# Performance work log

Measured on AMD Instinct MI355X. Metric: run time of the kernel, lower is better.

Reference implementation:

```python
import jax, jax.numpy as jnp
import numpy as np

EPS = 1e-07
NEG_DIAG = -10.0
HDCE_GAMMA = 1.0

def l2_normalize(x):
    # norm = (sum(x^2, axis=1))^(1/2); out = x / (norm + 1e-7)
    norm = jnp.sqrt(jnp.sum(x * x, axis=1, keepdims=True))
    return x / (norm + EPS)

def setup_inputs() -> dict:
    key = jax.random.key(0)
    k1, k2, k3 = jax.random.split(key, 3)
    N, D, DG = 4096, 256, 256
    feat_q = jax.random.normal(k1, (N, D), dtype=jnp.float32)
    feat_k = jax.random.normal(k2, (N, D), dtype=jnp.float32)
    feat_g = jax.random.normal(k3, (N, DG), dtype=jnp.float32)
    return {"feat_q": feat_q, "feat_k": feat_k, "feat_g": feat_g}

def reference(feat_q, feat_k, feat_g):
    N = feat_q.shape[0]
    fq = l2_normalize(feat_q)  # computed in original but unused for weight_out
    fk = l2_normalize(feat_k)
    fg = l2_normalize(feat_g)
    # batched self-similarity with batch_dim_for_bmm = 1 -> [1, N, N]
    spatial_k = jnp.einsum('nd,md->nm', fk, fk)[None]
    spatial_g = jnp.einsum('nd,md->nm', fg, fg)[None]
    spatial_kg = (spatial_k + 1.0 + EPS) / (spatial_g + 1.0 + EPS)
    diag = jnp.eye(N, dtype=bool)[None]  # [1, N, N]
    weight_seed = jnp.where(diag, NEG_DIAG, spatial_kg)
    weight_out = jax.nn.softmax(weight_seed / HDCE_GAMMA, axis=2)
    wmax = jnp.max(weight_out, axis=2, keepdims=True)
    return weight_out / wmax
```

## Files before the change

### kernel.cpp

```cpp
#include <hip/hip_runtime.h>
#include <hip/hip_bf16.h>
#include <cmath>

typedef __attribute__((ext_vector_type(8))) short short8;
typedef __attribute__((ext_vector_type(4))) float f32x4;

#define EPS_F 1e-7f
#define NEG_DIAG_F -10.0f

__device__ __forceinline__ unsigned enc_f32(float f) {
    unsigned u = __float_as_uint(f);
    return (u & 0x80000000u) ? ~u : (u | 0x80000000u);
}
__device__ __forceinline__ float dec_f32(unsigned u) {
    return (u & 0x80000000u) ? __uint_as_float(u ^ 0x80000000u) : __uint_as_float(~u);
}

__device__ __forceinline__ void gload_lds16(const void* gptr, void* ldsptr) {
    __builtin_amdgcn_global_load_lds(
        (const __attribute__((address_space(1))) unsigned int*)gptr,
        (__attribute__((address_space(3))) unsigned int*)ldsptr,
        16, 0, 0);
}

__global__ void norm_cast_kernel(const float* __restrict__ fk, const float* __restrict__ fg,
                                 __hip_bfloat16* __restrict__ fkb, __hip_bfloat16* __restrict__ fgb,
                                 unsigned* __restrict__ rowmax, int N, int D) {
    int n = blockIdx.x;
    int t = threadIdx.x;
    float xk = fk[(size_t)n * D + t];
    float xg = fg[(size_t)n * D + t];
    float sk = xk * xk, sg = xg * xg;
#pragma unroll
    for (int off = 32; off > 0; off >>= 1) {
        sk += __shfl_xor(sk, off, 64);
        sg += __shfl_xor(sg, off, 64);
    }
    __shared__ float lsk[4], lsg[4];
    int w = t >> 6, l = t & 63;
    if (l == 0) { lsk[w] = sk; lsg[w] = sg; }
    __syncthreads();
    sk = lsk[0] + lsk[1] + lsk[2] + lsk[3];
    sg = lsg[0] + lsg[1] + lsg[2] + lsg[3];
    float rkv = 1.0f / (sqrtf(sk) + EPS_F);
    float rgv = 1.0f / (sqrtf(sg) + EPS_F);
    fkb[(size_t)n * D + t] = __float2bfloat16(xk * rkv);
    fgb[(size_t)n * D + t] = __float2bfloat16(xg * rgv);
    if (t == 0) rowmax[n] = 0u;
}

#define BM 128
#define BN 128
#define BK 64
#define NTHREADS 512

__global__ __launch_bounds__(NTHREADS) void dual_gram_kernel(
    const __hip_bfloat16* __restrict__ fkb, const __hip_bfloat16* __restrict__ fgb,
    float* __restrict__ out, unsigned* __restrict__ rowmax, int N, int D) {

    __shared__ __align__(16) __hip_bfloat16 lAk[BM * BK];
    __shared__ __align__(16) __hip_bfloat16 lBk[BN * BK];
    __shared__ __align__(16) __hip_bfloat16 lAg[BM * BK];
    __shared__ __align__(16) __hip_bfloat16 lBg[BN * BK];

    int t = threadIdx.x;
    int ntiles = N / BN;
    int bid = blockIdx.x;
    int by = bid / ntiles, bx = bid % ntiles;
    int r0 = by * BM, c0 = bx * BN;

    int w = t >> 6, l = t & 63;
    int wr = w >> 2, wc = w & 3;
    int lr = l & 15, lg = l >> 4;

    f32x4 acck[4][2], accg[4][2];
    f32x4 zero = {0.f, 0.f, 0.f, 0.f};
#pragma unroll
    for (int m = 0; m < 4; ++m)
#pragma unroll
        for (int n = 0; n < 2; ++n) { acck[m][n] = zero; accg[m][n] = zero; }

    const size_t rowbytes = (size_t)D * 2;

    for (int k0 = 0; k0 < D; k0 += BK) {
#pragma unroll
        for (int c = 0; c < 2; ++c) {
            int o = (t + c * NTHREADS) * 16;
            int row = o >> 7;
            int csw = (o & 127) ^ ((row & 7) << 4);
            size_t goffA = (size_t)(r0 + row) * rowbytes + (size_t)k0 * 2 + csw;
            size_t goffB = (size_t)(c0 + row) * rowbytes + (size_t)k0 * 2 + csw;
            int ldsoff = (w << 10) + (c << 13);
            gload_lds16((const char*)fkb + goffA, (char*)lAk + ldsoff);
            gload_lds16((const char*)fkb + goffB, (char*)lBk + ldsoff);
            gload_lds16((const char*)fgb + goffA, (char*)lAg + ldsoff);
            gload_lds16((const char*)fgb + goffB, (char*)lBg + ldsoff);
        }
        __syncthreads();

#pragma unroll
        for (int kk = 0; kk < BK; kk += 32) {
            int kb = (kk + lg * 8) * 2;
            short8 ak[4], ag[4], bk2[2], bg2[2];
#pragma unroll
            for (int m = 0; m < 4; ++m) {
                int row = wr * 64 + m * 16 + lr;
                int o = (row << 7) + kb;
                o ^= ((row & 7) << 4);
                ak[m] = *(const short8*)((const char*)lAk + o);
                ag[m] = *(const short8*)((const char*)lAg + o);
            }
#pragma unroll
            for (int n = 0; n < 2; ++n) {
                int row = wc * 32 + n * 16 + lr;
                int o = (row << 7) + kb;
                o ^= ((row & 7) << 4);
                bk2[n] = *(const short8*)((const char*)lBk + o);
                bg2[n] = *(const short8*)((const char*)lBg + o);
            }
#pragma unroll
            for (int m = 0; m < 4; ++m)
#pragma unroll
                for (int n = 0; n < 2; ++n) {
                    acck[m][n] = __builtin_amdgcn_mfma_f32_16x16x32_bf16(ak[m], bk2[n], acck[m][n], 0, 0, 0);
                    accg[m][n] = __builtin_amdgcn_mfma_f32_16x16x32_bf16(ag[m], bg2[n], accg[m][n], 0, 0, 0);
                }
        }
        __syncthreads();
    }

    int gcoln[2];
#pragma unroll
    for (int n = 0; n < 2; ++n) gcoln[n] = c0 + wc * 32 + n * 16 + lr;

#pragma unroll
    for (int m = 0; m < 4; ++m) {
#pragma unroll
        for (int j = 0; j < 4; ++j) {
            int grow = r0 + wr * 64 + m * 16 + lg * 4 + j;
            float pm = NEG_DIAG_F;
#pragma unroll
            for (int n = 0; n < 2; ++n) {
                float dk = acck[m][n][j];
                float dg = accg[m][n][j];
                float s = (dk + 1.0f + EPS_F) / (dg + 1.0f + EPS_F);
                if (grow == gcoln[n]) s = NEG_DIAG_F;
                out[(size_t)grow * N + gcoln[n]] = s;
                pm = fmaxf(pm, s);
            }
#pragma unroll
            for (int off = 1; off < 16; off <<= 1)
                pm = fmaxf(pm, __shfl_xor(pm, off, 64));
            if (lr == 0) atomicMax(&rowmax[grow], enc_f32(pm));
        }
    }
}

__global__ void finalize_kernel(float* __restrict__ out, const unsigned* __restrict__ rowmax, int N) {
    size_t total = (size_t)N * N / 4;
    int cols4 = N / 4;
    size_t stride = (size_t)gridDim.x * blockDim.x;
    for (size_t i = (size_t)blockIdx.x * blockDim.x + threadIdx.x; i < total; i += stride) {
        float4 v = reinterpret_cast<float4*>(out)[i];
        int row = (int)(i / cols4);
        float m = dec_f32(rowmax[row]);
        v.x = __expf(v.x - m);
        v.y = __expf(v.y - m);
        v.z = __expf(v.z - m);
        v.w = __expf(v.w - m);
        reinterpret_cast<float4*>(out)[i] = v;
    }
}

extern "C" void kernel_launch(void* const* d_in, const int* in_sizes, int n_in,
                              void* d_out, int out_size, void* d_ws, size_t ws_size,
                              hipStream_t stream) {
    const float* fk = (const float*)d_in[1];
    const float* fg = (const float*)d_in[2];
    float* out = (float*)d_out;

    int N = (int)llround(sqrt((double)out_size));
    int D = in_sizes[1] / N;

    char* ws = (char*)d_ws;
    __hip_bfloat16* fkb = (__hip_bfloat16*)ws;
    __hip_bfloat16* fgb = (__hip_bfloat16*)(ws + (size_t)N * D * 2);
    unsigned* rowmax = (unsigned*)(ws + (size_t)N * D * 4);

    norm_cast_kernel<<<N, D, 0, stream>>>(fk, fg, fkb, fgb, rowmax, N, D);

    int nt = N / BN;
    dual_gram_kernel<<<nt * nt, NTHREADS, 0, stream>>>(fkb, fgb, out, rowmax, N, D);

    finalize_kernel<<<2048, 256, 0, stream>>>(out, rowmax, N);
}
```

Before: 77.71 us.

## Double-buffer gram tiles with BK=32, swizzle workgroup order, cheaper divide and indexing

Restructures the dual-gram main loop into a double-buffered LDS pipeline with BK=32. The next k-slice is prefetched via global_load_lds while MFMAs run on the current one, using a new XOR swizzle and precomputed LDS offsets. It also remaps block IDs so consecutive workgroups land on different tile rows, raises wave priority around MFMAs, and replaces the fp32 divide with a hardware reciprocal. The finalize row index now uses a shift, which is only correct when N/4 is a power of two, and the reciprocal slightly changes rounding.

```diff
diff --git a/kernel.cpp b/kernel.cpp
--- a/kernel.cpp
+++ b/kernel.cpp
@@ -51,21 +51,21 @@
 
 #define BM 128
 #define BN 128
-#define BK 64
+#define BK 32
 #define NTHREADS 512
+#define TILE_B (BM * BK * 2)
+#define BUF_B  (4 * TILE_B)
 
 __global__ __launch_bounds__(NTHREADS) void dual_gram_kernel(
     const __hip_bfloat16* __restrict__ fkb, const __hip_bfloat16* __restrict__ fgb,
     float* __restrict__ out, unsigned* __restrict__ rowmax, int N, int D) {
 
-    __shared__ __align__(16) __hip_bfloat16 lAk[BM * BK];
-    __shared__ __align__(16) __hip_bfloat16 lBk[BN * BK];
-    __shared__ __align__(16) __hip_bfloat16 lAg[BM * BK];
-    __shared__ __align__(16) __hip_bfloat16 lBg[BN * BK];
+    __shared__ __align__(16) char smem[2 * BUF_B];
 
     int t = threadIdx.x;
     int ntiles = N / BN;
-    int bid = blockIdx.x;
+    int nwg = ntiles * ntiles;
+    int bid = (blockIdx.x & 7) * (nwg >> 3) + (blockIdx.x >> 3);
     int by = bid / ntiles, bx = bid % ntiles;
     int r0 = by * BM, c0 = bx * BN;
 
@@ -73,6 +73,26 @@
     int wr = w >> 2, wc = w & 3;
     int lr = l & 15, lg = l >> 4;
 
+    int srow = t >> 2;
+    int sslot = t & 3;
+    int scsb = ((sslot ^ ((srow >> 1) & 3)) << 4);
+    const size_t rowbytes = (size_t)D * 2;
+    size_t gA = (size_t)(r0 + srow) * rowbytes + scsb;
+    size_t gB = (size_t)(c0 + srow) * rowbytes + scsb;
+    int ldst = t << 4;
+
+    int aoff[4], boff[2];
+#pragma unroll
+    for (int m = 0; m < 4; ++m) {
+        int row = wr * 64 + m * 16 + lr;
+        aoff[m] = row * 64 + (((lg ^ ((row >> 1) & 3))) << 4);
+    }
+#pragma unroll
+    for (int n = 0; n < 2; ++n) {
+        int row = wc * 32 + n * 16 + lr;
+        boff[n] = row * 64 + (((lg ^ ((row >> 1) & 3))) << 4);
+    }
+
     f32x4 acck[4][2], accg[4][2];
     f32x4 zero = {0.f, 0.f, 0.f, 0.f};
 #pragma unroll
@@ -80,52 +100,47 @@
 #pragma unroll
         for (int n = 0; n < 2; ++n) { acck[m][n] = zero; accg[m][n] = zero; }
 
-    const size_t rowbytes = (size_t)D * 2;
-
-    for (int k0 = 0; k0 < D; k0 += BK) {
-#pragma unroll
-        for (int c = 0; c < 2; ++c) {
-            int o = (t + c * NTHREADS) * 16;
-            int row = o >> 7;
-            int csw = (o & 127) ^ ((row & 7) << 4);
-            size_t goffA = (size_t)(r0 + row) * rowbytes + (size_t)k0 * 2 + csw;
-            size_t goffB = (size_t)(c0 + row) * rowbytes + (size_t)k0 * 2 + csw;
-            int ldsoff = (w << 10) + (c << 13);
-            gload_lds16((const char*)fkb + goffA, (char*)lAk + ldsoff);
-            gload_lds16((const char*)fkb + goffB, (char*)lBk + ldsoff);
-            gload_lds16((const char*)fgb + goffA, (char*)lAg + ldsoff);
-            gload_lds16((const char*)fgb + goffB, (char*)lBg + ldsoff);
-        }
-        __syncthreads();
-
-#pragma unroll
-        for (int kk = 0; kk < BK; kk += 32) {
-            int kb = (kk + lg * 8) * 2;
-            short8 ak[4], ag[4], bk2[2], bg2[2];
-#pragma unroll
-            for (int m = 0; m < 4; ++m) {
-                int row = wr * 64 + m * 16 + lr;
-                int o = (row << 7) + kb;
-                o ^= ((row & 7) << 4);
-                ak[m] = *(const short8*)((const char*)lAk + o);
-                ag[m] = *(const short8*)((const char*)lAg + o);
+    int ksteps = D / BK;
+
+    {
+        gload_lds16((const char*)fkb + gA, smem + 0 * TILE_B + ldst);
+        gload_lds16((const char*)fkb + gB, smem + 1 * TILE_B + ldst);
+        gload_lds16((const char*)fgb + gA, smem + 2 * TILE_B + ldst);
+        gload_lds16((const char*)fgb + gB, smem + 3 * TILE_B + ldst);
+    }
+    __syncthreads();
+
+    for (int ks = 0; ks < ksteps; ++ks) {
+        int cur = ks & 1;
+        if (ks + 1 < ksteps) {
+            size_t kb = (size_t)(ks + 1) * (BK * 2);
+            char* dst = smem + (cur ^ 1) * BUF_B + ldst;
+            gload_lds16((const char*)fkb + gA + kb, dst + 0 * TILE_B);
+            gload_lds16((const char*)fkb + gB + kb, dst + 1 * TILE_B);
+            gload_lds16((const char*)fgb + gA + kb, dst + 2 * TILE_B);
+            gload_lds16((const char*)fgb + gB + kb, dst + 3 * TILE_B);
+        }
+        const char* base = smem + cur * BUF_B;
+        short8 ak[4], ag[4], bk2[2], bg2[2];
+#pragma unroll
+        for (int m = 0; m < 4; ++m) {
+            ak[m] = *(const short8*)(base + 0 * TILE_B + aoff[m]);
+            ag[m] = *(const short8*)(base + 2 * TILE_B + aoff[m]);
+        }
+#pragma unroll
+        for (int n = 0; n < 2; ++n) {
+            bk2[n] = *(const short8*)(base + 1 * TILE_B + boff[n]);
+            bg2[n] = *(const short8*)(base + 3 * TILE_B + boff[n]);
+        }
+        __builtin_amdgcn_s_setprio(1);
+#pragma unroll
+        for (int m = 0; m < 4; ++m)
+#pragma unroll
+            for (int n = 0; n < 2; ++n) {
+                acck[m][n] = __builtin_amdgcn_mfma_f32_16x16x32_bf16(ak[m], bk2[n], acck[m][n], 0, 0, 0);
+                accg[m][n] = __builtin_amdgcn_mfma_f32_16x16x32_bf16(ag[m], bg2[n], accg[m][n], 0, 0, 0);
             }
-#pragma unroll
-            for (int n = 0; n < 2; ++n) {
-                int row = wc * 32 + n * 16 + lr;
-                int o = (row << 7) + kb;
-                o ^= ((row & 7) << 4);
-                bk2[n] = *(const short8*)((const char*)lBk + o);
-                bg2[n] = *(const short8*)((const char*)lBg + o);
-            }
-#pragma unroll
-            for (int m = 0; m < 4; ++m)
-#pragma unroll
-                for (int n = 0; n < 2; ++n) {
-                    acck[m][n] = __builtin_amdgcn_mfma_f32_16x16x32_bf16(ak[m], bk2[n], acck[m][n], 0, 0, 0);
-                    accg[m][n] = __builtin_amdgcn_mfma_f32_16x16x32_bf16(ag[m], bg2[n], accg[m][n], 0, 0, 0);
-                }
-        }
+        __builtin_amdgcn_s_setprio(0);
         __syncthreads();
     }
 
@@ -143,7 +158,7 @@
             for (int n = 0; n < 2; ++n) {
                 float dk = acck[m][n][j];
                 float dg = accg[m][n][j];
-                float s = (dk + 1.0f + EPS_F) / (dg + 1.0f + EPS_F);
+                float s = (dk + 1.0f + EPS_F) * __builtin_amdgcn_rcpf(dg + 1.0f + EPS_F);
                 if (grow == gcoln[n]) s = NEG_DIAG_F;
                 out[(size_t)grow * N + gcoln[n]] = s;
                 pm = fmaxf(pm, s);
@@ -158,11 +173,12 @@
 
 __global__ void finalize_kernel(float* __restrict__ out, const unsigned* __restrict__ rowmax, int N) {
     size_t total = (size_t)N * N / 4;
-    int cols4 = N / 4;
+    int cols4 = N >> 2;
+    int sh = 31 - __clz(cols4);
     size_t stride = (size_t)gridDim.x * blockDim.x;
     for (size_t i = (size_t)blockIdx.x * blockDim.x + threadIdx.x; i < total; i += stride) {
         float4 v = reinterpret_cast<float4*>(out)[i];
-        int row = (int)(i / cols4);
+        int row = (int)(i >> sh);
         float m = dec_f32(rowmax[row]);
         v.x = __expf(v.x - m);
         v.y = __expf(v.y - m);
```

Result: slower. 105.8 us (+36.2%).

## Exploit Gram symmetry, stage output through LDS, replace global atomics with partial maxima

Applied to the files above, without the earlier changes.

The dual Gram kernel now computes only upper-triangular tiles and writes each off-diagonal tile both directly and transposed, halving the MFMA work. Stores go through a padded LDS bounce buffer so they become coalesced float4 writes. Row maxima are reduced per block in LDS and written as per-tile partials to a workspace array, which removes global atomics and the rowmax init. Finalize then runs one block per row, reducing the 32 partials itself. Division becomes a hardware reciprocal, trading a little accuracy, and the transposed store costs extra LDS traffic and syncs.

```diff
diff --git a/kernel.cpp b/kernel.cpp
--- a/kernel.cpp
+++ b/kernel.cpp
@@ -8,13 +8,12 @@
 #define EPS_F 1e-7f
 #define NEG_DIAG_F -10.0f
 
-__device__ __forceinline__ unsigned enc_f32(float f) {
-    unsigned u = __float_as_uint(f);
-    return (u & 0x80000000u) ? ~u : (u | 0x80000000u);
-}
-__device__ __forceinline__ float dec_f32(unsigned u) {
-    return (u & 0x80000000u) ? __uint_as_float(u ^ 0x80000000u) : __uint_as_float(~u);
-}
+#define BM 128
+#define BN 128
+#define BK 64
+#define NTHREADS 512
+#define PADW 132
+#define NPART 32
 
 __device__ __forceinline__ void gload_lds16(const void* gptr, void* ldsptr) {
     __builtin_amdgcn_global_load_lds(
@@ -25,7 +24,7 @@
 
 __global__ void norm_cast_kernel(const float* __restrict__ fk, const float* __restrict__ fg,
                                  __hip_bfloat16* __restrict__ fkb, __hip_bfloat16* __restrict__ fgb,
-                                 unsigned* __restrict__ rowmax, int N, int D) {
+                                 int N, int D) {
     int n = blockIdx.x;
     int t = threadIdx.x;
     float xk = fk[(size_t)n * D + t];
@@ -46,32 +45,29 @@
     float rgv = 1.0f / (sqrtf(sg) + EPS_F);
     fkb[(size_t)n * D + t] = __float2bfloat16(xk * rkv);
     fgb[(size_t)n * D + t] = __float2bfloat16(xg * rgv);
-    if (t == 0) rowmax[n] = 0u;
-}
-
-#define BM 128
-#define BN 128
-#define BK 64
-#define NTHREADS 512
+}
 
 __global__ __launch_bounds__(NTHREADS) void dual_gram_kernel(
     const __hip_bfloat16* __restrict__ fkb, const __hip_bfloat16* __restrict__ fgb,
-    float* __restrict__ out, unsigned* __restrict__ rowmax, int N, int D) {
-
-    __shared__ __align__(16) __hip_bfloat16 lAk[BM * BK];
-    __shared__ __align__(16) __hip_bfloat16 lBk[BN * BK];
-    __shared__ __align__(16) __hip_bfloat16 lAg[BM * BK];
-    __shared__ __align__(16) __hip_bfloat16 lBg[BN * BK];
+    float* __restrict__ out, float* __restrict__ P, int N, int D) {
+
+    __shared__ __align__(16) char smem[PADW * 128 * 4 + 1024];
+    float* bounce = (float*)smem;
+    int* lmax = (int*)(smem + PADW * 128 * 4);
+
+    int bx = blockIdx.x, by = blockIdx.y;
+    if (by > bx) return;
+    int r0 = by * BM, c0 = bx * BN;
 
     int t = threadIdx.x;
-    int ntiles = N / BN;
-    int bid = blockIdx.x;
-    int by = bid / ntiles, bx = bid % ntiles;
-    int r0 = by * BM, c0 = bx * BN;
-
     int w = t >> 6, l = t & 63;
     int wr = w >> 2, wc = w & 3;
     int lr = l & 15, lg = l >> 4;
+
+    char* lAk = smem;
+    char* lBk = smem + 16384;
+    char* lAg = smem + 32768;
+    char* lBg = smem + 49152;
 
     f32x4 acck[4][2], accg[4][2];
     f32x4 zero = {0.f, 0.f, 0.f, 0.f};
@@ -91,10 +87,10 @@
             size_t goffA = (size_t)(r0 + row) * rowbytes + (size_t)k0 * 2 + csw;
             size_t goffB = (size_t)(c0 + row) * rowbytes + (size_t)k0 * 2 + csw;
             int ldsoff = (w << 10) + (c << 13);
-            gload_lds16((const char*)fkb + goffA, (char*)lAk + ldsoff);
-            gload_lds16((const char*)fkb + goffB, (char*)lBk + ldsoff);
-            gload_lds16((const char*)fgb + goffA, (char*)lAg + ldsoff);
-            gload_lds16((const char*)fgb + goffB, (char*)lBg + ldsoff);
+            gload_lds16((const char*)fkb + goffA, lAk + ldsoff);
+            gload_lds16((const char*)fkb + goffB, lBk + ldsoff);
+            gload_lds16((const char*)fgb + goffA, lAg + ldsoff);
+            gload_lds16((const char*)fgb + goffB, lBg + ldsoff);
         }
         __syncthreads();
 
@@ -107,16 +103,16 @@
                 int row = wr * 64 + m * 16 + lr;
                 int o = (row << 7) + kb;
                 o ^= ((row & 7) << 4);
-                ak[m] = *(const short8*)((const char*)lAk + o);
-                ag[m] = *(const short8*)((const char*)lAg + o);
+                ak[m] = *(const short8*)(lAk + o);
+                ag[m] = *(const short8*)(lAg + o);
             }
 #pragma unroll
             for (int n = 0; n < 2; ++n) {
                 int row = wc * 32 + n * 16 + lr;
                 int o = (row << 7) + kb;
                 o ^= ((row & 7) << 4);
-                bk2[n] = *(const short8*)((const char*)lBk + o);
-                bg2[n] = *(const short8*)((const char*)lBg + o);
+                bk2[n] = *(const short8*)(lBk + o);
+                bg2[n] = *(const short8*)(lBg + o);
             }
 #pragma unroll
             for (int m = 0; m < 4; ++m)
@@ -129,46 +125,108 @@
         __syncthreads();
     }
 
-    int gcoln[2];
-#pragma unroll
-    for (int n = 0; n < 2; ++n) gcoln[n] = c0 + wc * 32 + n * 16 + lr;
-
-#pragma unroll
-    for (int m = 0; m < 4; ++m) {
+    if (t < 256) lmax[t] = 0;
+
+    int lcol[2];
+#pragma unroll
+    for (int n = 0; n < 2; ++n) lcol[n] = wc * 32 + n * 16 + lr;
+
+#pragma unroll
+    for (int m = 0; m < 4; ++m)
 #pragma unroll
         for (int j = 0; j < 4; ++j) {
-            int grow = r0 + wr * 64 + m * 16 + lg * 4 + j;
-            float pm = NEG_DIAG_F;
+            int lrow = wr * 64 + m * 16 + lg * 4 + j;
 #pragma unroll
             for (int n = 0; n < 2; ++n) {
                 float dk = acck[m][n][j];
                 float dg = accg[m][n][j];
-                float s = (dk + 1.0f + EPS_F) / (dg + 1.0f + EPS_F);
-                if (grow == gcoln[n]) s = NEG_DIAG_F;
-                out[(size_t)grow * N + gcoln[n]] = s;
-                pm = fmaxf(pm, s);
+                float s = (dk + 1.0f + EPS_F) * __builtin_amdgcn_rcpf(dg + 1.0f + EPS_F);
+                if (r0 + lrow == c0 + lcol[n]) s = NEG_DIAG_F;
+                acck[m][n][j] = s;
             }
+        }
+    __syncthreads();
+
+#pragma unroll
+    for (int m = 0; m < 4; ++m)
+#pragma unroll
+        for (int j = 0; j < 4; ++j) {
+            float pm = fmaxf(acck[m][0][j], acck[m][1][j]);
 #pragma unroll
             for (int off = 1; off < 16; off <<= 1)
                 pm = fmaxf(pm, __shfl_xor(pm, off, 64));
-            if (lr == 0) atomicMax(&rowmax[grow], enc_f32(pm));
-        }
-    }
-}
-
-__global__ void finalize_kernel(float* __restrict__ out, const unsigned* __restrict__ rowmax, int N) {
-    size_t total = (size_t)N * N / 4;
-    int cols4 = N / 4;
-    size_t stride = (size_t)gridDim.x * blockDim.x;
-    for (size_t i = (size_t)blockIdx.x * blockDim.x + threadIdx.x; i < total; i += stride) {
-        float4 v = reinterpret_cast<float4*>(out)[i];
-        int row = (int)(i / cols4);
-        float m = dec_f32(rowmax[row]);
+            if (lr == 0) atomicMax(&lmax[wr * 64 + m * 16 + lg * 4 + j], __float_as_int(pm));
+        }
+#pragma unroll
+    for (int n = 0; n < 2; ++n) {
+        float cm = acck[0][n][0];
+#pragma unroll
+        for (int m = 0; m < 4; ++m)
+#pragma unroll
+            for (int j = 0; j < 4; ++j) cm = fmaxf(cm, acck[m][n][j]);
+        cm = fmaxf(cm, __shfl_xor(cm, 16, 64));
+        cm = fmaxf(cm, __shfl_xor(cm, 32, 64));
+        if (l < 16) atomicMax(&lmax[128 + lcol[n]], __float_as_int(cm));
+    }
+
+#pragma unroll
+    for (int m = 0; m < 4; ++m)
+#pragma unroll
+        for (int n = 0; n < 2; ++n)
+#pragma unroll
+            for (int j = 0; j < 4; ++j)
+                bounce[(wr * 64 + m * 16 + lg * 4 + j) * PADW + lcol[n]] = acck[m][n][j];
+    __syncthreads();
+
+#pragma unroll
+    for (int i = 0; i < 8; ++i) {
+        int r = (t >> 5) + 16 * i;
+        int k = t & 31;
+        f32x4 v = *(const f32x4*)(bounce + r * PADW + 4 * k);
+        *(f32x4*)(out + (size_t)(r0 + r) * N + c0 + 4 * k) = v;
+    }
+    if (t < 128) {
+        P[(size_t)(r0 + t) * NPART + bx] = __int_as_float(lmax[t]);
+    } else if (t < 256 && by != bx) {
+        P[(size_t)(c0 + t - 128) * NPART + by] = __int_as_float(lmax[t]);
+    }
+
+    if (by != bx) {
+        __syncthreads();
+#pragma unroll
+        for (int m = 0; m < 4; ++m)
+#pragma unroll
+            for (int n = 0; n < 2; ++n)
+#pragma unroll
+                for (int j = 0; j < 4; ++j)
+                    bounce[lcol[n] * PADW + (wr * 64 + m * 16 + lg * 4 + j)] = acck[m][n][j];
+        __syncthreads();
+#pragma unroll
+        for (int i = 0; i < 8; ++i) {
+            int cc = (t >> 5) + 16 * i;
+            int k = t & 31;
+            f32x4 v = *(const f32x4*)(bounce + cc * PADW + 4 * k);
+            *(f32x4*)(out + (size_t)(c0 + cc) * N + r0 + 4 * k) = v;
+        }
+    }
+}
+
+__global__ void finalize_kernel(float* __restrict__ out, const float* __restrict__ P, int N) {
+    int row = blockIdx.x;
+    int t = threadIdx.x;
+    float m = P[(size_t)row * NPART + (t & 31)];
+#pragma unroll
+    for (int off = 1; off < 32; off <<= 1)
+        m = fmaxf(m, __shfl_xor(m, off, 64));
+    float4* o4 = (float4*)(out + (size_t)row * N);
+    int n4 = N >> 2;
+    for (int i = t; i < n4; i += 256) {
+        float4 v = o4[i];
         v.x = __expf(v.x - m);
         v.y = __expf(v.y - m);
         v.z = __expf(v.z - m);
         v.w = __expf(v.w - m);
-        reinterpret_cast<float4*>(out)[i] = v;
+        o4[i] = v;
     }
 }
 
@@ -183,14 +241,14 @@
     int D = in_sizes[1] / N;
 
     char* ws = (char*)d_ws;
-    __hip_bfloat16* fkb = (__hip_bfloat16*)ws;
-    __hip_bfloat16* fgb = (__hip_bfloat16*)(ws + (size_t)N * D * 2);
-    unsigned* rowmax = (unsigned*)(ws + (size_t)N * D * 4);
-
-    norm_cast_kernel<<<N, D, 0, stream>>>(fk, fg, fkb, fgb, rowmax, N, D);
+    float* P = (float*)ws;
+    __hip_bfloat16* fkb = (__hip_bfloat16*)(ws + (size_t)N * NPART * 4);
+    __hip_bfloat16* fgb = (__hip_bfloat16*)(ws + (size_t)N * NPART * 4 + (size_t)N * D * 2);
+
+    norm_cast_kernel<<<N, D, 0, stream>>>(fk, fg, fkb, fgb, N, D);
 
     int nt = N / BN;
-    dual_gram_kernel<<<nt * nt, NTHREADS, 0, stream>>>(fkb, fgb, out, rowmax, N, D);
-
-    finalize_kernel<<<2048, 256, 0, stream>>>(out, rowmax, N);
-}
+    dual_gram_kernel<<<dim3(nt, nt), NTHREADS, 0, stream>>>(fkb, fgb, out, P, N, D);
+
+    finalize_kernel<<<N, 256, 0, stream>>>(out, P, N);
+}
```

Result: faster. 65.60 us (-15.6%).
